# Performance work log

Measured on AMD Instinct MI355X. Metric: run time of the kernel, lower is better.

The kernel has to match this reference:

```python
import jax, jax.numpy as jnp
import numpy as np

GRID = 16777216
X_MIN, X_MAX = -10.0, 10.0
DX = (X_MAX - X_MIN) / (GRID - 1)
DT = 0.01
STEPS = 100


def setup_inputs() -> dict:
    key = jax.random.key(0)
    k1, k2 = jax.random.split(key)
    psi = jax.random.normal(k1, (GRID, 2), dtype=jnp.float32)
    noise = jax.random.normal(k2, (STEPS,), dtype=jnp.float32)
    x = jnp.linspace(X_MIN, X_MAX, GRID, dtype=jnp.float32).reshape(-1, 1)
    c0 = GRID // 2  # fixed start index (torch.randint in original)
    return {"psi": psi, "noise": noise, "x": x, "c0": c0}


def reference(psi, noise, x, c0):
    # --- density and score on the 1D grid ---
    psi = jnp.nan_to_num(psi, nan=0.0, posinf=1.0, neginf=-1.0)
    prob = psi[:, 0] ** 2 + psi[:, 1] ** 2                      # [GRID]
    prob = prob / (jnp.sum(prob) * DX + 1e-8)
    prob = jnp.clip(prob, 1e-12)
    log_prob = jnp.log(prob)
    # central finite-difference score, zero at boundaries
    score = jnp.zeros_like(log_prob).at[1:-1].set(
        (log_prob[2:] - log_prob[:-2]) / (2.0 * DX))
    score = jnp.nan_to_num(score)

    # --- sequential Langevin walk over the grid index ---
    sqrt_2dt = np.sqrt(2.0 * DT).astype(np.float32)

    def step(c_idx, n):
        s = score[c_idx]
        move = s * DT + n * sqrt_2dt
        move = jnp.where(jnp.isfinite(move), move, 0.0)
        shift = (move / DX).astype(jnp.int32)  # int() truncation toward zero
        c_idx = jnp.clip(c_idx + shift, 0, GRID - 1)
        return c_idx, None

    c_final, _ = jax.lax.scan(step, jnp.int32(c0), noise)
    return x[c_final]  # shape [1]
```

## Files before the change

### kernel.cpp

```cpp
#include <hip/hip_runtime.h>
#include <cstdint>
#include <climits>

#define GRID_N 16777216
#define GMAX (GRID_N - 1)
#define N_STEPS 100
#define NCAND (2 * N_STEPS + 1)
#define NNODE (2 * N_STEPS)
#define NLEV 8
#define NBLK 2048
#define THREADS 256
#define TTOT (NBLK * THREADS)

#define TERM_FLAG 0x40000000
#define FALLBACK  (-1)

__device__ __forceinline__ float fixv(float v) {
    if (isnan(v)) return 0.0f;
    if (isinf(v)) return v > 0.0f ? 1.0f : -1.0f;
    return v;
}

__device__ __forceinline__ float raw_prob(float a, float b) {
    return __fadd_rn(__fmul_rn(a, a), __fmul_rn(b, b));
}

__device__ __forceinline__ int host_f2i(float sf) {
    if (!(sf >= -2147483648.0f && sf < 2147483648.0f)) return INT_MIN;
    return (int)sf;
}

__device__ __forceinline__ int wrap_clip(int c, int shift) {
    int r = (int)((unsigned)c + (unsigned)shift);
    if (r < 0) r = 0;
    if (r > GMAX) r = GMAX;
    return r;
}

__device__ __forceinline__ double pair_prob(float4 v) {
    return (double)raw_prob(fixv(v.x), fixv(v.y)) +
           (double)raw_prob(fixv(v.z), fixv(v.w));
}

__global__ __launch_bounds__(256) void qpe_sum_kernel(const float4* __restrict__ psi4,
                                                      double* __restrict__ partials) {
    const int tid = threadIdx.x;
    int i = blockIdx.x * THREADS + tid;
    double a0 = 0.0, a1 = 0.0, a2 = 0.0, a3 = 0.0;
#pragma unroll
    for (int k = 0; k < 4; ++k) {
        float4 v0 = psi4[i];
        float4 v1 = psi4[i + TTOT];
        float4 v2 = psi4[i + 2 * TTOT];
        float4 v3 = psi4[i + 3 * TTOT];
        i += 4 * TTOT;
        a0 += pair_prob(v0);
        a1 += pair_prob(v1);
        a2 += pair_prob(v2);
        a3 += pair_prob(v3);
    }
    double acc = (a0 + a1) + (a2 + a3);
    __shared__ double sm[256];
    sm[tid] = acc;
    __syncthreads();
    for (int s = 128; s > 0; s >>= 1) {
        if (tid < s) sm[tid] += sm[tid + s];
        __syncthreads();
    }
    if (tid == 0) partials[blockIdx.x] = sm[0];
}

__global__ __launch_bounds__(256) void qpe_walk_kernel(const float* __restrict__ psi,
                                                       const float* __restrict__ noise,
                                                       const float* __restrict__ x,
                                                       const int* __restrict__ c0p,
                                                       const double* __restrict__ partials,
                                                       float* __restrict__ out) {
    const int tid = threadIdx.x;
    const float DXf    = (float)(20.0 / (double)(GRID_N - 1));
    const float TWODXf = (float)(2.0 * (20.0 / (double)(GRID_N - 1)));
    const float DTf    = 0.01f;
    const float SQ2DTf = (float)0.14142135623730950488;

    __shared__ int    cand_c[256];
    __shared__ int    cand_next[256];
    __shared__ int    lift[NLEV][NNODE];
    __shared__ double red[256];
    __shared__ float  norm_sh;

    int myc = -1;
    float2 lo = make_float2(0.0f, 0.0f), hi = make_float2(0.0f, 0.0f);
    if (tid < NCAND) {
        if (tid == NCAND - 1) {
            myc = *c0p;
        } else {
            int t = tid >> 1;
            float n = noise[t];
            float move = __fadd_rn(__fmul_rn(0.0f, DTf), __fmul_rn(n, SQ2DTf));
            if (!isfinite(move)) move = 0.0f;
            int shift = host_f2i(__fdiv_rn(move, DXf));
            int b = (tid & 1) ? GMAX : 0;
            myc = wrap_clip(b, shift);
        }
        if (myc > 0 && myc < GMAX) {
            lo = *(const float2*)(psi + 2 * myc - 2);
            hi = *(const float2*)(psi + 2 * myc + 2);
        }
        asm volatile("" : "+v"(lo.x), "+v"(lo.y), "+v"(hi.x), "+v"(hi.y));
    }

    double acc = 0.0;
#pragma unroll
    for (int k = 0; k < NBLK / 256; ++k) acc += partials[tid + k * 256];
    red[tid] = acc;
    __syncthreads();
    for (int s = 128; s > 0; s >>= 1) {
        if (tid < s) red[tid] += red[tid + s];
        __syncthreads();
    }
    if (tid == 0) {
        float S = (float)red[0];
        norm_sh = __fadd_rn(__fmul_rn(S, DXf), 1e-8f);
    }
    __syncthreads();
    float norm = norm_sh;

    float s_val = 0.0f;
    int nxt = -2;
    if (tid < NCAND && myc > 0 && myc < GMAX) {
        float a0 = fixv(lo.x), b0 = fixv(lo.y);
        float a1 = fixv(hi.x), b1 = fixv(hi.y);
        float p1 = fmaxf(__fdiv_rn(raw_prob(a1, b1), norm), 1e-12f);
        float p0 = fmaxf(__fdiv_rn(raw_prob(a0, b0), norm), 1e-12f);
        s_val = __fdiv_rn(__fsub_rn(logf(p1), logf(p0)), TWODXf);
        int nidx = (tid == NCAND - 1) ? 0 : (tid >> 1) + 1;
        if (nidx < N_STEPS) {
            float n = noise[nidx];
            float move = __fadd_rn(__fmul_rn(s_val, DTf), __fmul_rn(n, SQ2DTf));
            if (!isfinite(move)) move = 0.0f;
            int shift = host_f2i(__fdiv_rn(move, DXf));
            nxt = wrap_clip(myc, shift);
        }
    }
    cand_c[tid] = (tid < NCAND) ? myc : -1;
    cand_next[tid] = nxt;
    if (tid < NCAND) {
        float w = x[myc < 0 ? 0 : myc];
        float w2 = x[(nxt < 0) ? 0 : nxt];
        asm volatile("" :: "v"(w), "v"(w2));
    }
    __syncthreads();

    if (tid < NNODE) {
        int t = tid >> 1;
        int v;
        int c1 = cand_c[tid];
        if (c1 == 0 || c1 == GMAX) {
            int t1 = t + 1;
            v = (t1 == N_STEPS) ? (TERM_FLAG | c1) : ((t1 << 1) | (c1 == GMAX));
        } else if (t + 1 == N_STEPS) {
            v = TERM_FLAG | c1;
        } else {
            int c2 = cand_next[tid];
            if (c2 == 0 || c2 == GMAX) {
                int t2 = t + 2;
                v = (t2 == N_STEPS) ? (TERM_FLAG | c2) : ((t2 << 1) | (c2 == GMAX));
            } else if (t + 2 == N_STEPS) {
                v = TERM_FLAG | c2;
            } else {
                v = FALLBACK;
            }
        }
        lift[0][tid] = v;
    }
    __syncthreads();
#pragma unroll
    for (int k = 1; k < NLEV; ++k) {
        if (tid < NNODE) {
            int v = lift[k - 1][tid];
            lift[k][tid] = (v >= 0 && v < TERM_FLAG) ? lift[k - 1][v] : v;
        }
        __syncthreads();
    }

    if (tid != 0) return;

    int c = cand_c[NCAND - 1];
    int t = 0;
    bool need_serial = false;

    int node;
    if (c == 0 || c == GMAX) {
        node = (0 << 1) | (c == GMAX);
    } else {
        int n1 = cand_next[NCAND - 1];
        if (n1 == -2) { need_serial = true; node = -1; }
        else if (n1 == 0 || n1 == GMAX) {
            if (N_STEPS == 1) { out[0] = x[n1]; return; }
            node = (1 << 1) | (n1 == GMAX);
        } else if (N_STEPS == 1) {
            out[0] = x[n1]; return;
        } else {
            need_serial = true; t = 1; c = n1; node = -1;
        }
    }

    if (!need_serial) {
        for (int guard = 0; guard < 64; ++guard) {
            if (node >= TERM_FLAG) break;
            int applied = 0;
            for (int k = NLEV - 1; k >= 0; --k) {
                int v = lift[k][node];
                if (v != FALLBACK) {
                    node = v;
                    applied = 1;
                    break;
                }
            }
            if (!applied) {
                t = node >> 1;
                c = (node & 1) ? GMAX : 0;
                need_serial = true;
                break;
            }
            if (node >= TERM_FLAG) break;
        }
        if (!need_serial && node >= TERM_FLAG) {
            out[0] = x[node & 0xFFFFFF];
            return;
        }
    }

    while (t < N_STEPS) {
        if (c <= 0 || c >= GMAX) {
            int j = 2 * t + ((c != 0) ? 1 : 0);
            c = cand_c[j];
            ++t;
        } else {
            float a1v = fixv(psi[2 * (c + 1)]);
            float b1v = fixv(psi[2 * (c + 1) + 1]);
            float a0v = fixv(psi[2 * (c - 1)]);
            float b0v = fixv(psi[2 * (c - 1) + 1]);
            float p1 = fmaxf(__fdiv_rn(raw_prob(a1v, b1v), norm), 1e-12f);
            float p0 = fmaxf(__fdiv_rn(raw_prob(a0v, b0v), norm), 1e-12f);
            float s = __fdiv_rn(__fsub_rn(logf(p1), logf(p0)), TWODXf);
            float n = noise[t];
            float move = __fadd_rn(__fmul_rn(s, DTf), __fmul_rn(n, SQ2DTf));
            if (!isfinite(move)) move = 0.0f;
            int shift = host_f2i(__fdiv_rn(move, DXf));
            c = wrap_clip(c, shift);
            ++t;
        }
    }
    out[0] = x[c];
}

extern "C" void kernel_launch(void* const* d_in, const int* in_sizes, int n_in,
                              void* d_out, int out_size, void* d_ws, size_t ws_size,
                              hipStream_t stream) {
    const float* psi   = (const float*)d_in[0];
    const float* noise = (const float*)d_in[1];
    const float* x     = (const float*)d_in[2];
    const int*   c0    = (const int*)d_in[3];
    float* out = (float*)d_out;

    double* partials = (double*)d_ws;

    qpe_sum_kernel<<<NBLK, THREADS, 0, stream>>>((const float4*)psi, partials);
    qpe_walk_kernel<<<1, THREADS, 0, stream>>>(psi, noise, x, c0, partials, out);
}
```

Baseline: 34.73 us.

## Move candidate psi gathers into an extra block of the sum kernel

Adds one extra block to the reduction kernel that computes the 201 candidate start positions and gathers their neighbouring psi values into a workspace buffer. The single-block walk kernel then reads these contiguously instead of issuing scattered gathers on its own critical path. The reduction loop is also restructured to issue 8 independent float4 loads per iteration instead of 4. The cost is an extra workspace buffer and an extra pass over candidate positions.

```diff
diff --git a/kernel.cpp b/kernel.cpp
--- a/kernel.cpp
+++ b/kernel.cpp
@@ -15,6 +15,8 @@
 #define TERM_FLAG 0x40000000
 #define FALLBACK  (-1)
 
+#define GATH_OFF 16384
+
 __device__ __forceinline__ float fixv(float v) {
     if (isnan(v)) return 0.0f;
     if (isinf(v)) return v > 0.0f ? 1.0f : -1.0f;
@@ -42,24 +44,69 @@
            (double)raw_prob(fixv(v.z), fixv(v.w));
 }
 
+__device__ __forceinline__ int cand_pos(int tid, const float* noise,
+                                        const int* c0p, float DXf, float DTf,
+                                        float SQ2DTf) {
+    if (tid == NCAND - 1) return *c0p;
+    int t = tid >> 1;
+    float n = noise[t];
+    float move = __fadd_rn(__fmul_rn(0.0f, DTf), __fmul_rn(n, SQ2DTf));
+    if (!isfinite(move)) move = 0.0f;
+    int shift = host_f2i(__fdiv_rn(move, DXf));
+    int b = (tid & 1) ? GMAX : 0;
+    return wrap_clip(b, shift);
+}
+
 __global__ __launch_bounds__(256) void qpe_sum_kernel(const float4* __restrict__ psi4,
-                                                      double* __restrict__ partials) {
+                                                      double* __restrict__ partials,
+                                                      const float* __restrict__ psi,
+                                                      const float* __restrict__ noise,
+                                                      const int* __restrict__ c0p,
+                                                      float4* __restrict__ gath) {
     const int tid = threadIdx.x;
-    int i = blockIdx.x * THREADS + tid;
+    const int bid = blockIdx.x;
+
+    if (bid == NBLK) {
+        const float DXf    = (float)(20.0 / (double)(GRID_N - 1));
+        const float DTf    = 0.01f;
+        const float SQ2DTf = (float)0.14142135623730950488;
+        if (tid < NCAND) {
+            int myc = cand_pos(tid, noise, c0p, DXf, DTf, SQ2DTf);
+            float4 g = make_float4(0.0f, 0.0f, 0.0f, 0.0f);
+            if (myc > 0 && myc < GMAX) {
+                float2 lo = *(const float2*)(psi + 2 * myc - 2);
+                float2 hi = *(const float2*)(psi + 2 * myc + 2);
+                g = make_float4(lo.x, lo.y, hi.x, hi.y);
+            }
+            gath[tid] = g;
+        }
+        return;
+    }
+
+    int i = bid * THREADS + tid;
     double a0 = 0.0, a1 = 0.0, a2 = 0.0, a3 = 0.0;
+    double a4 = 0.0, a5 = 0.0, a6 = 0.0, a7 = 0.0;
 #pragma unroll
-    for (int k = 0; k < 4; ++k) {
+    for (int k = 0; k < 2; ++k) {
         float4 v0 = psi4[i];
         float4 v1 = psi4[i + TTOT];
         float4 v2 = psi4[i + 2 * TTOT];
         float4 v3 = psi4[i + 3 * TTOT];
-        i += 4 * TTOT;
+        float4 v4 = psi4[i + 4 * TTOT];
+        float4 v5 = psi4[i + 5 * TTOT];
+        float4 v6 = psi4[i + 6 * TTOT];
+        float4 v7 = psi4[i + 7 * TTOT];
+        i += 8 * TTOT;
         a0 += pair_prob(v0);
         a1 += pair_prob(v1);
         a2 += pair_prob(v2);
         a3 += pair_prob(v3);
-    }
-    double acc = (a0 + a1) + (a2 + a3);
+        a4 += pair_prob(v4);
+        a5 += pair_prob(v5);
+        a6 += pair_prob(v6);
+        a7 += pair_prob(v7);
+    }
+    double acc = ((a0 + a1) + (a2 + a3)) + ((a4 + a5) + (a6 + a7));
     __shared__ double sm[256];
     sm[tid] = acc;
     __syncthreads();
@@ -67,7 +114,7 @@
         if (tid < s) sm[tid] += sm[tid + s];
         __syncthreads();
     }
-    if (tid == 0) partials[blockIdx.x] = sm[0];
+    if (tid == 0) partials[bid] = sm[0];
 }
 
 __global__ __launch_bounds__(256) void qpe_walk_kernel(const float* __restrict__ psi,
@@ -75,6 +122,7 @@
                                                        const float* __restrict__ x,
                                                        const int* __restrict__ c0p,
                                                        const double* __restrict__ partials,
+                                                       const float4* __restrict__ gath,
                                                        float* __restrict__ out) {
     const int tid = threadIdx.x;
     const float DXf    = (float)(20.0 / (double)(GRID_N - 1));
@@ -89,24 +137,11 @@
     __shared__ float  norm_sh;
 
     int myc = -1;
-    float2 lo = make_float2(0.0f, 0.0f), hi = make_float2(0.0f, 0.0f);
+    float4 g = make_float4(0.0f, 0.0f, 0.0f, 0.0f);
     if (tid < NCAND) {
-        if (tid == NCAND - 1) {
-            myc = *c0p;
-        } else {
-            int t = tid >> 1;
-            float n = noise[t];
-            float move = __fadd_rn(__fmul_rn(0.0f, DTf), __fmul_rn(n, SQ2DTf));
-            if (!isfinite(move)) move = 0.0f;
-            int shift = host_f2i(__fdiv_rn(move, DXf));
-            int b = (tid & 1) ? GMAX : 0;
-            myc = wrap_clip(b, shift);
-        }
-        if (myc > 0 && myc < GMAX) {
-            lo = *(const float2*)(psi + 2 * myc - 2);
-            hi = *(const float2*)(psi + 2 * myc + 2);
-        }
-        asm volatile("" : "+v"(lo.x), "+v"(lo.y), "+v"(hi.x), "+v"(hi.y));
+        myc = cand_pos(tid, noise, c0p, DXf, DTf, SQ2DTf);
+        g = gath[tid];
+        asm volatile("" : "+v"(g.x), "+v"(g.y), "+v"(g.z), "+v"(g.w));
     }
 
     double acc = 0.0;
@@ -128,8 +163,8 @@
     float s_val = 0.0f;
     int nxt = -2;
     if (tid < NCAND && myc > 0 && myc < GMAX) {
-        float a0 = fixv(lo.x), b0 = fixv(lo.y);
-        float a1 = fixv(hi.x), b1 = fixv(hi.y);
+        float a0 = fixv(g.x), b0 = fixv(g.y);
+        float a1 = fixv(g.z), b1 = fixv(g.w);
         float p1 = fmaxf(__fdiv_rn(raw_prob(a1, b1), norm), 1e-12f);
         float p0 = fmaxf(__fdiv_rn(raw_prob(a0, b0), norm), 1e-12f);
         s_val = __fdiv_rn(__fsub_rn(logf(p1), logf(p0)), TWODXf);
@@ -265,7 +300,10 @@
     float* out = (float*)d_out;
 
     double* partials = (double*)d_ws;
-
-    qpe_sum_kernel<<<NBLK, THREADS, 0, stream>>>((const float4*)psi, partials);
-    qpe_walk_kernel<<<1, THREADS, 0, stream>>>(psi, noise, x, c0, partials, out);
-}
+    float4* gath = (float4*)((char*)d_ws + GATH_OFF);
+
+    qpe_sum_kernel<<<NBLK + 1, THREADS, 0, stream>>>((const float4*)psi, partials,
+                                                     psi, noise, c0, gath);
+    qpe_walk_kernel<<<1, THREADS, 0, stream>>>(psi, noise, x, c0, partials,
+                                               gath, out);
+}
```

Measured after the change: 35.32 us. Within noise of the previous version (+1.7%).
